# Kernel optimization log

Measured on AMD Instinct MI355X. Metric: run time of the kernel, lower is better.

Reference implementation:

```python
import jax, jax.numpy as jnp
import numpy as np


def setup_inputs() -> dict:
    key = jax.random.key(0)
    k1, k2 = jax.random.split(key)
    B, Tq, Tk, D = 8, 2048, 2048, 1024
    query = jax.random.normal(k1, (B, Tq, D), dtype=jnp.float32)
    key_t = jax.random.normal(k2, (B, Tk, D), dtype=jnp.float32)
    return {"query": query, "key": key_t}


def reference(query, key):
    # Unscaled cross attention: key acts as both K and V.
    # energy: [B, Tq, Tk]
    energy = jnp.einsum("bqd,bkd->bqk", query, key)
    attention = jax.nn.softmax(energy, axis=-1)
    # output: [B, Tq, D]
    return jnp.einsum("bqk,bkd->bqd", attention, key)
```

## Files before the change

### kernel.cpp

```cpp
#include <hip/hip_runtime.h>
#include <stdint.h>

typedef int i32x4 __attribute__((ext_vector_type(4)));
typedef int8_t s8;

__device__ __forceinline__ void gload_lds16(const void* g, uint32_t lds_addr) {
  __builtin_amdgcn_global_load_lds(
      (const __attribute__((address_space(1))) void*)(uintptr_t)g,
      (__attribute__((address_space(3))) void*)(uintptr_t)lds_addr,
      16, 0, 0);
}

__device__ __forceinline__ void qsplit(float x, float s, float sinv, float s2inv,
                                       int& q1, int& q2) {
  float a = rintf(x * sinv);
  a = fminf(fmaxf(a, -127.f), 127.f);
  float r = fmaf(a, -s, x);
  float b = fminf(fmaxf(rintf(r * s2inv), -127.f), 127.f);
  q1 = (int)a; q2 = (int)b;
}
__device__ __forceinline__ uint32_t pack4(int b0, int b1, int b2, int b3) {
  return ((uint32_t)(uint8_t)b0) | ((uint32_t)(uint8_t)b1 << 8) |
         ((uint32_t)(uint8_t)b2 << 16) | ((uint32_t)(uint8_t)b3 << 24);
}

#define SQ (8.0f / 127.0f)
#define SQ_INV 15.875f
#define SQ2_INV 2032.0f

__global__ __launch_bounds__(256) void cvt_q_i8(const float* __restrict__ x,
                                                s8* __restrict__ a, s8* __restrict__ b) {
  size_t i = ((size_t)blockIdx.x * 256 + threadIdx.x) * 8;
  float4 v0 = ((const float4*)(x + i))[0];
  float4 v1 = ((const float4*)(x + i))[1];
  float f[8] = {v0.x, v0.y, v0.z, v0.w, v1.x, v1.y, v1.z, v1.w};
  int q1[8], q2[8];
#pragma unroll
  for (int j = 0; j < 8; j++) qsplit(f[j], SQ, SQ_INV, SQ2_INV, q1[j], q2[j]);
  uint2 ua, ub;
  ua.x = pack4(q1[0], q1[1], q1[2], q1[3]); ua.y = pack4(q1[4], q1[5], q1[6], q1[7]);
  ub.x = pack4(q2[0], q2[1], q2[2], q2[3]); ub.y = pack4(q2[4], q2[5], q2[6], q2[7]);
  *(uint2*)(a + i) = ua;
  *(uint2*)(b + i) = ub;
}

__global__ __launch_bounds__(256) void cvt_k_i8(const float* __restrict__ K,
                                                s8* __restrict__ k1, s8* __restrict__ k2,
                                                s8* __restrict__ t1, s8* __restrict__ t2) {
  __shared__ uint32_t tile[64][33];
  const int b = blockIdx.z;
  const int d0 = blockIdx.x * 32, t0 = blockIdx.y * 64;
  const int tid = threadIdx.x;
  const float* Kb = K + (size_t)b * 2048 * 1024;
  {
    const int t = tid >> 2, d8 = (tid & 3) * 8;
    const float* src = Kb + (size_t)(t0 + t) * 1024 + d0 + d8;
    float4 v0 = ((const float4*)src)[0];
    float4 v1 = ((const float4*)src)[1];
    float f[8] = {v0.x, v0.y, v0.z, v0.w, v1.x, v1.y, v1.z, v1.w};
    int q1[8], q2[8];
#pragma unroll
    for (int j = 0; j < 8; j++) {
      qsplit(f[j], SQ, SQ_INV, SQ2_INV, q1[j], q2[j]);
      tile[t][d8 + j] = ((uint32_t)(uint8_t)q1[j]) | ((uint32_t)(uint8_t)q2[j] << 8);
    }
    uint2 ua, ub;
    ua.x = pack4(q1[0], q1[1], q1[2], q1[3]); ua.y = pack4(q1[4], q1[5], q1[6], q1[7]);
    ub.x = pack4(q2[0], q2[1], q2[2], q2[3]); ub.y = pack4(q2[4], q2[5], q2[6], q2[7]);
    size_t off = (size_t)b * 2048 * 1024 + (size_t)(t0 + t) * 1024 + d0 + d8;
    *(uint2*)(k1 + off) = ua;
    *(uint2*)(k2 + off) = ub;
  }
  __syncthreads();
  {
    const int d = tid >> 3, tg = tid & 7;
    uint32_t v[8];
#pragma unroll
    for (int i = 0; i < 8; i++) v[i] = tile[tg * 8 + i][d];
    uint2 ua, ub;
    ua.x = pack4(v[0], v[1], v[2], v[3]); ua.y = pack4(v[4], v[5], v[6], v[7]);
    ub.x = pack4(v[0] >> 8, v[1] >> 8, v[2] >> 8, v[3] >> 8);
    ub.y = pack4(v[4] >> 8, v[5] >> 8, v[6] >> 8, v[7] >> 8);
    size_t off = (size_t)b * 1024 * 2048 + (size_t)(d0 + d) * 2048 + t0 + tg * 8;
    *(uint2*)(t1 + off) = ua;
    *(uint2*)(t2 + off) = ub;
  }
}

__global__ __launch_bounds__(256) void softmax_i8(const float* __restrict__ E,
                                                  s8* __restrict__ P1, s8* __restrict__ P2) {
  const size_t row = blockIdx.x;
  const float* e = E + row * 2048;
  const int t = threadIdx.x;
  float4 a = ((const float4*)e)[t * 2];
  float4 b = ((const float4*)e)[t * 2 + 1];
  float f[8] = {a.x, a.y, a.z, a.w, b.x, b.y, b.z, b.w};
  float m = f[0];
#pragma unroll
  for (int j = 1; j < 8; j++) m = fmaxf(m, f[j]);
#pragma unroll
  for (int off = 32; off > 0; off >>= 1) m = fmaxf(m, __shfl_down(m, off));
  __shared__ float redm[4], reds[4];
  if ((t & 63) == 0) redm[t >> 6] = m;
  __syncthreads();
  m = fmaxf(fmaxf(redm[0], redm[1]), fmaxf(redm[2], redm[3]));
  float ex[8];
  float s = 0.f;
#pragma unroll
  for (int j = 0; j < 8; j++) { ex[j] = __expf(f[j] - m); s += ex[j]; }
#pragma unroll
  for (int off = 32; off > 0; off >>= 1) s += __shfl_down(s, off);
  if ((t & 63) == 0) reds[t >> 6] = s;
  __syncthreads();
  s = reds[0] + reds[1] + reds[2] + reds[3];
  float inv = 1.0f / s;
  int q1[8], q2[8];
#pragma unroll
  for (int j = 0; j < 8; j++)
    qsplit(ex[j] * inv, 1.0f / 127.0f, 127.0f, 16256.0f, q1[j], q2[j]);
  uint2 ua, ub;
  ua.x = pack4(q1[0], q1[1], q1[2], q1[3]); ua.y = pack4(q1[4], q1[5], q1[6], q1[7]);
  ub.x = pack4(q2[0], q2[1], q2[2], q2[3]); ub.y = pack4(q2[4], q2[5], q2[6], q2[7]);
  *(uint2*)(P1 + row * 2048 + t * 8) = ua;
  *(uint2*)(P2 + row * 2048 + t * 8) = ub;
}

__global__ __launch_bounds__(256, 2) void gemm_i8(
    const s8* __restrict__ A0, const s8* __restrict__ A1,
    const s8* __restrict__ B0, const s8* __restrict__ B1,
    float* __restrict__ C, int Kdim, int ldc, long sA, long sB, long sC,
    float c1, float c2) {
  __shared__ char lds[2][32768];
  const int tid = threadIdx.x;
  const int w = tid >> 6, l = tid & 63;

  const int gx = gridDim.x, gy = gridDim.y;
  const int nwg = gx * gy * gridDim.z;
  const int f = (blockIdx.z * gy + blockIdx.y) * gx + blockIdx.x;
  const int cpx = nwg >> 3;
  const int swz = (f & 7) * cpx + (f >> 3);
  const int bandsz = 8 * gy;
  const int band = swz / bandsz, r = swz % bandsz;
  const int nbx = gx >> 3;
  const int bx = (band % nbx) * 8 + (r & 7);
  const int by = r >> 3;
  const int bz = band / nbx;

  const int rowA = by * 128, rowB = bx * 128;
  const s8* bases[4] = {A0 + bz * sA, A1 + bz * sA, B0 + bz * sB, B1 + bz * sB};
  const int rbase[4] = {rowA, rowA, rowB, rowB};
  const s8* gp[8];
  uint32_t lpo[8];
#pragma unroll
  for (int i = 0; i < 8; i++) {
    int gc = w * 8 + i;
    int buf = gc >> 3, c = gc & 7;
    int row = c * 16 + (l >> 2);
    int q = (l & 3) ^ ((row >> 1) & 3);
    gp[i] = bases[buf] + (size_t)(rbase[buf] + row) * Kdim + q * 16;
    lpo[i] = (uint32_t)(uintptr_t)(&lds[0][0] + buf * 8192 + c * 1024 + l * 16);
  }
  i32x4 acc1[4][4], acc2[4][4];
  const i32x4 zero = {0, 0, 0, 0};
#pragma unroll
  for (int mt = 0; mt < 4; mt++)
#pragma unroll
    for (int nt = 0; nt < 4; nt++) { acc1[mt][nt] = zero; acc2[mt][nt] = zero; }

  const int wm = w & 1, wn = w >> 1, q4 = l >> 4, rl = l & 15;

#pragma unroll
  for (int i = 0; i < 8; i++) { gload_lds16(gp[i], lpo[i]); gp[i] += 64; }

#define STAGE2(i0, i1)                                         \
  do {                                                         \
    gload_lds16(gp[i0], lpo[i0] + nb); gp[i0] += 64;           \
    gload_lds16(gp[i1], lpo[i1] + nb); gp[i1] += 64;           \
  } while (0)

#define GPHASE(p, STAGE_STMT)                                                  \
  {                                                                            \
    int row_ = wn * 64 + (p) * 16 + rl;                                        \
    int off_ = row_ * 64 + ((q4 ^ ((row_ >> 1) & 3)) << 4);                    \
    i32x4 bf0 = *(const i32x4*)(L + 16384 + off_);                             \
    i32x4 bf1 = *(const i32x4*)(L + 24576 + off_);                             \
    if (pf) { STAGE_STMT; }                                                    \
    asm volatile("s_waitcnt lgkmcnt(0)" ::: "memory");                         \
    __builtin_amdgcn_sched_barrier(0);                                         \
    __builtin_amdgcn_s_setprio(1);                                             \
    _Pragma("unroll")                                                          \
    for (int mt = 0; mt < 4; mt++) {                                           \
      acc1[mt][p] = __builtin_amdgcn_mfma_i32_16x16x64_i8(af0[mt], bf0, acc1[mt][p], 0, 0, 0); \
      acc2[mt][p] = __builtin_amdgcn_mfma_i32_16x16x64_i8(af0[mt], bf1, acc2[mt][p], 0, 0, 0); \
      acc2[mt][p] = __builtin_amdgcn_mfma_i32_16x16x64_i8(af1[mt], bf0, acc2[mt][p], 0, 0, 0); \
    }                                                                          \
    __builtin_amdgcn_s_setprio(0);                                             \
  }

  int cur = 0;
  for (int k0 = 0; k0 < Kdim; k0 += 64) {
    const bool pf = (k0 + 64 < Kdim);
    const uint32_t nb = (uint32_t)(cur ^ 1) * 32768u;
    __builtin_amdgcn_s_barrier();
    if (pf) {
      STAGE2(0, 1);
      asm volatile("s_waitcnt vmcnt(2)" ::: "memory");
    } else {
      asm volatile("s_waitcnt vmcnt(0)" ::: "memory");
    }
    __builtin_amdgcn_sched_barrier(0);
    __builtin_amdgcn_s_barrier();
    __builtin_amdgcn_sched_barrier(0);
    const char* L = &lds[cur][0];
    i32x4 af0[4], af1[4];
#pragma unroll
    for (int mt = 0; mt < 4; mt++) {
      int row = wm * 64 + mt * 16 + rl;
      int off = row * 64 + ((q4 ^ ((row >> 1) & 3)) << 4);
      af0[mt] = *(const i32x4*)(L + off);
      af1[mt] = *(const i32x4*)(L + 8192 + off);
    }
    GPHASE(0, STAGE2(2, 3));
    __builtin_amdgcn_s_barrier();
    GPHASE(1, STAGE2(4, 5));
    __builtin_amdgcn_s_barrier();
    GPHASE(2, STAGE2(6, 7));
    __builtin_amdgcn_s_barrier();
    GPHASE(3, ((void)0));
    cur ^= 1;
  }
#undef GPHASE
#undef STAGE2
  float* Cb = C + (size_t)bz * sC + (size_t)rowA * ldc + rowB;
#pragma unroll
  for (int mt = 0; mt < 4; mt++)
#pragma unroll
    for (int nt = 0; nt < 4; nt++)
#pragma unroll
      for (int r2 = 0; r2 < 4; r2++)
        Cb[(size_t)(wm * 64 + mt * 16 + q4 * 4 + r2) * ldc + (wn * 64 + nt * 16 + rl)] =
            c1 * (float)acc1[mt][nt][r2] + c2 * (float)acc2[mt][nt][r2];
}

extern "C" void kernel_launch(void* const* d_in, const int* in_sizes, int n_in,
                              void* d_out, int out_size, void* d_ws, size_t ws_size,
                              hipStream_t stream) {
  (void)in_sizes; (void)n_in; (void)out_size;
  const float* Q = (const float*)d_in[0];
  const float* K = (const float*)d_in[1];
  float* O = (float*)d_out;
  const int Btot = 8, Tq = 2048, Tk = 2048, D = 1024;
  const size_t perb = 36ull << 20;
  int NB = 8;
  while (NB > 1 && (size_t)NB * perb > ws_size) NB >>= 1;

  char* p = (char*)d_ws;
  const size_t qd = (size_t)NB * Tq * D;
  const size_t kd = (size_t)NB * Tk * D;
  const size_t ee = (size_t)NB * Tq * Tk;
  s8* Q1 = (s8*)p; p += qd;
  s8* Q2 = (s8*)p; p += qd;
  s8* K1 = (s8*)p; p += kd;
  s8* K2 = (s8*)p; p += kd;
  s8* KT1 = (s8*)p; p += kd;
  s8* KT2 = (s8*)p; p += kd;
  float* E = (float*)p; p += ee * 4;
  s8* P1 = (s8*)p; p += ee;
  s8* P2 = (s8*)p; p += ee;

  const float g1c1 = 64.0f / 16129.0f, g1c2 = g1c1 * (1.0f / 128.0f);
  const float g2c1 = 8.0f / 16129.0f, g2c2 = g2c1 * (1.0f / 128.0f);

  for (int c = 0; c < Btot / NB; c++) {
    const float* Qc = Q + (size_t)c * qd;
    const float* Kc = K + (size_t)c * kd;
    float* Oc = O + (size_t)c * qd;
    cvt_q_i8<<<dim3(NB * 1024), 256, 0, stream>>>(Qc, Q1, Q2);
    cvt_k_i8<<<dim3(32, 32, NB), 256, 0, stream>>>(Kc, K1, K2, KT1, KT2);
    gemm_i8<<<dim3(16, 16, NB), 256, 0, stream>>>(
        Q1, Q2, K1, K2, E, 1024, 2048, (long)Tq * D, (long)Tk * D, (long)Tq * Tk,
        g1c1, g1c2);
    softmax_i8<<<dim3(NB * Tq), 256, 0, stream>>>(E, P1, P2);
    gemm_i8<<<dim3(8, 16, NB), 256, 0, stream>>>(
        P1, P2, KT1, KT2, Oc, 2048, 1024, (long)Tq * Tk, (long)D * Tk, (long)Tq * D,
        g2c1, g2c2);
  }
}
```

Baseline: 386.1 us.

## Fuse Q and K int8 conversion kernels and halve batch chunk size

Merges the separate Q and K quantization kernels into one launch, with the extra grid rows handling Q. Drops the clamps in the softmax probability quantization, since probabilities in [0,1] cannot exceed the int8 range. Lowers the default batch chunk from 8 to 4, so the pipeline runs twice with smaller workspace buffers, likely for better cache residency of the energy matrix. This trades one kernel launch saved for twice as many launches overall.

```diff
diff --git a/kernel.cpp b/kernel.cpp
--- a/kernel.cpp
+++ b/kernel.cpp
@@ -28,29 +28,30 @@
 #define SQ_INV 15.875f
 #define SQ2_INV 2032.0f
 
-__global__ __launch_bounds__(256) void cvt_q_i8(const float* __restrict__ x,
-                                                s8* __restrict__ a, s8* __restrict__ b) {
-  size_t i = ((size_t)blockIdx.x * 256 + threadIdx.x) * 8;
-  float4 v0 = ((const float4*)(x + i))[0];
-  float4 v1 = ((const float4*)(x + i))[1];
-  float f[8] = {v0.x, v0.y, v0.z, v0.w, v1.x, v1.y, v1.z, v1.w};
-  int q1[8], q2[8];
-#pragma unroll
-  for (int j = 0; j < 8; j++) qsplit(f[j], SQ, SQ_INV, SQ2_INV, q1[j], q2[j]);
-  uint2 ua, ub;
-  ua.x = pack4(q1[0], q1[1], q1[2], q1[3]); ua.y = pack4(q1[4], q1[5], q1[6], q1[7]);
-  ub.x = pack4(q2[0], q2[1], q2[2], q2[3]); ub.y = pack4(q2[4], q2[5], q2[6], q2[7]);
-  *(uint2*)(a + i) = ua;
-  *(uint2*)(b + i) = ub;
-}
-
-__global__ __launch_bounds__(256) void cvt_k_i8(const float* __restrict__ K,
-                                                s8* __restrict__ k1, s8* __restrict__ k2,
-                                                s8* __restrict__ t1, s8* __restrict__ t2) {
+__global__ __launch_bounds__(256) void cvt_qk_i8(
+    const float* __restrict__ Q, s8* __restrict__ qa, s8* __restrict__ qb,
+    const float* __restrict__ K, s8* __restrict__ k1, s8* __restrict__ k2,
+    s8* __restrict__ t1, s8* __restrict__ t2) {
   __shared__ uint32_t tile[64][33];
   const int b = blockIdx.z;
+  const int tid = threadIdx.x;
+  if (blockIdx.y >= 32) {
+    size_t c = (size_t)(blockIdx.y - 32) * 32 + blockIdx.x;
+    size_t i = (((size_t)b * 1024 + c) * 256 + tid) * 8;
+    float4 v0 = ((const float4*)(Q + i))[0];
+    float4 v1 = ((const float4*)(Q + i))[1];
+    float f[8] = {v0.x, v0.y, v0.z, v0.w, v1.x, v1.y, v1.z, v1.w};
+    int q1[8], q2[8];
+#pragma unroll
+    for (int j = 0; j < 8; j++) qsplit(f[j], SQ, SQ_INV, SQ2_INV, q1[j], q2[j]);
+    uint2 ua, ub;
+    ua.x = pack4(q1[0], q1[1], q1[2], q1[3]); ua.y = pack4(q1[4], q1[5], q1[6], q1[7]);
+    ub.x = pack4(q2[0], q2[1], q2[2], q2[3]); ub.y = pack4(q2[4], q2[5], q2[6], q2[7]);
+    *(uint2*)(qa + i) = ua;
+    *(uint2*)(qb + i) = ub;
+    return;
+  }
   const int d0 = blockIdx.x * 32, t0 = blockIdx.y * 64;
-  const int tid = threadIdx.x;
   const float* Kb = K + (size_t)b * 2048 * 1024;
   {
     const int t = tid >> 2, d8 = (tid & 3) * 8;
@@ -116,8 +117,13 @@
   float inv = 1.0f / s;
   int q1[8], q2[8];
 #pragma unroll
-  for (int j = 0; j < 8; j++)
-    qsplit(ex[j] * inv, 1.0f / 127.0f, 127.0f, 16256.0f, q1[j], q2[j]);
+  for (int j = 0; j < 8; j++) {
+    float x = ex[j] * inv;
+    float qa = rintf(x * 127.0f);
+    float r = fmaf(qa, -1.0f / 127.0f, x);
+    float qb = rintf(r * 16256.0f);
+    q1[j] = (int)qa; q2[j] = (int)qb;
+  }
   uint2 ua, ub;
   ua.x = pack4(q1[0], q1[1], q1[2], q1[3]); ua.y = pack4(q1[4], q1[5], q1[6], q1[7]);
   ub.x = pack4(q2[0], q2[1], q2[2], q2[3]); ub.y = pack4(q2[4], q2[5], q2[6], q2[7]);
@@ -251,7 +257,7 @@
   float* O = (float*)d_out;
   const int Btot = 8, Tq = 2048, Tk = 2048, D = 1024;
   const size_t perb = 36ull << 20;
-  int NB = 8;
+  int NB = 4;
   while (NB > 1 && (size_t)NB * perb > ws_size) NB >>= 1;
 
   char* p = (char*)d_ws;
@@ -275,8 +281,7 @@
     const float* Qc = Q + (size_t)c * qd;
     const float* Kc = K + (size_t)c * kd;
     float* Oc = O + (size_t)c * qd;
-    cvt_q_i8<<<dim3(NB * 1024), 256, 0, stream>>>(Qc, Q1, Q2);
-    cvt_k_i8<<<dim3(32, 32, NB), 256, 0, stream>>>(Kc, K1, K2, KT1, KT2);
+    cvt_qk_i8<<<dim3(32, 64, NB), 256, 0, stream>>>(Qc, Q1, Q2, Kc, K1, K2, KT1, KT2);
     gemm_i8<<<dim3(16, 16, NB), 256, 0, stream>>>(
         Q1, Q2, K1, K2, E, 1024, 2048, (long)Tq * D, (long)Tk * D, (long)Tq * Tk,
         g1c1, g1c2);
```

After: 391.5 us. No clear change (+1.4%).
